# Performance work log

Hardware: AMD Instinct MI355X
Metric: run time of the kernel (lower is better)

Reference implementation:

```python
import jax, jax.numpy as jnp
import numpy as np
import math

DIM = 2048
N_HEADS = 16
N_KV_HEADS = 8
HEAD_DIM = DIM // N_HEADS  # 128
N_REP = N_HEADS // N_KV_HEADS  # 2
BLOCK = 128
TOPK = 8
NEG_INF = -10000.0
SEQ = 4096
BS = 1


def _rope_tables(seq_len, head_dim, base=10000.0):
    inv_freq = 1.0 / (base ** (jnp.arange(0, head_dim, 2, dtype=jnp.float32) / head_dim))
    ang = jnp.arange(seq_len, dtype=jnp.float32)[:, None] * inv_freq[None, :]  # [S, hd/2]
    return jnp.cos(ang), jnp.sin(ang)


def _apply_rope(t, cos, sin):
    # t: [bs, S, h, hd]; interleaved pairs
    t1 = t[..., 0::2]
    t2 = t[..., 1::2]
    c = cos[None, :, None, :]
    s = sin[None, :, None, :]
    out_even = t1 * c - t2 * s
    out_odd = t1 * s + t2 * c
    out = jnp.stack([out_even, out_odd], axis=-1)  # [bs,S,h,hd/2,2]
    return out.reshape(t.shape)


def setup_inputs() -> dict:
    key = jax.random.key(0)
    ks = jax.random.split(key, 5)
    scale = 1.0 / math.sqrt(DIM)
    x = jax.random.normal(ks[0], (BS, SEQ, DIM), dtype=jnp.float32)
    wq = jax.random.normal(ks[1], (DIM, N_HEADS * HEAD_DIM), dtype=jnp.float32) * scale
    wk = jax.random.normal(ks[2], (DIM, N_KV_HEADS * HEAD_DIM), dtype=jnp.float32) * scale
    wv = jax.random.normal(ks[3], (DIM, N_KV_HEADS * HEAD_DIM), dtype=jnp.float32) * scale
    wo = jax.random.normal(ks[4], (DIM, DIM), dtype=jnp.float32) * scale
    return {"x": x, "wq": wq, "wk": wk, "wv": wv, "wo": wo}


def reference(x, wq, wk, wv, wo):
    bs, S, _ = x.shape
    inv_sqrt_d = 1.0 / math.sqrt(HEAD_DIM)

    q = (x @ wq).reshape(bs, S, N_HEADS, HEAD_DIM)
    k = (x @ wk).reshape(bs, S, N_KV_HEADS, HEAD_DIM)
    v = (x @ wv).reshape(bs, S, N_KV_HEADS, HEAD_DIM)

    cos, sin = _rope_tables(S, HEAD_DIM)
    q = _apply_rope(q, cos, sin)
    k = _apply_rope(k, cos, sin)

    # [bs, h, S, hd]
    q = jnp.transpose(q, (0, 2, 1, 3))
    k = jnp.transpose(k, (0, 2, 1, 3))
    v = jnp.transpose(v, (0, 2, 1, 3))

    # GQA expand (repeat_interleave over head dim)
    k_e = jnp.repeat(k, N_REP, axis=1)
    v_e = jnp.repeat(v, N_REP, axis=1)

    num_blocks = S // BLOCK  # 32, divides evenly (pad_len == 0)
    k_blocks = k_e.reshape(bs, N_HEADS, num_blocks, BLOCK, HEAD_DIM)
    block_means = k_blocks.mean(axis=3)  # [bs,h,nb,hd]

    gating = jnp.einsum('bhsd,bhnd->bhsn', q, block_means) * inv_sqrt_d
    q_block_idx = jnp.arange(S) // BLOCK
    future_block = q_block_idx[:, None] < jnp.arange(num_blocks)[None, :]  # [S, nb]
    gating = jnp.where(future_block[None, None], NEG_INF, gating)

    curr_k = min(TOPK, num_blocks)
    _, sel_idx = jax.lax.top_k(gating, curr_k)  # [bs,h,S,k]
    selected = jnp.sum(jax.nn.one_hot(sel_idx, num_blocks, dtype=jnp.float32), axis=-2) > 0  # [bs,h,S,nb]

    token_keep = jnp.repeat(selected, BLOCK, axis=-1)[..., :S]  # [bs,h,S,S]
    token_mask = jnp.where(token_keep, 0.0, NEG_INF)

    scores = jnp.einsum('bhsd,bhtd->bhst', q, k_e) * inv_sqrt_d
    causal = jnp.triu(jnp.ones((S, S), dtype=jnp.float32), k=1)  # 1 where future token
    # faithful to source: elementwise max of token mask and causal*neg_inf
    final_mask = jnp.maximum(token_mask, causal[None, None] * NEG_INF)
    scores = scores + final_mask

    probs = jax.nn.softmax(scores.astype(jnp.float32), axis=-1).astype(scores.dtype)
    out = jnp.einsum('bhst,bhtd->bhsd', probs, v_e)
    out = jnp.transpose(out, (0, 2, 1, 3)).reshape(bs, S, N_HEADS * HEAD_DIM)
    return out @ wo
```

## Files before the change

kernel.cpp:

```cpp
#include <hip/hip_runtime.h>
#include <hip/hip_fp16.h>

#define SQ   4096
#define DIMM 2048
#define QKVN 4096

typedef unsigned short u16;
typedef unsigned int u32;
typedef __attribute__((ext_vector_type(8))) short    short8;
typedef __attribute__((ext_vector_type(8))) _Float16 half8;
typedef __attribute__((ext_vector_type(4))) float    f32x4;

__device__ __forceinline__ u16 f2bf(float f) {
  u32 u = __float_as_uint(f);
  u32 r = u + 0x7fffu + ((u >> 16) & 1u);
  return (u16)(r >> 16);
}
__device__ __forceinline__ float bf2f(u16 h) { return __uint_as_float(((u32)h) << 16); }
__device__ __forceinline__ u16 f2h(float f) { return __half_as_ushort(__float2half(f)); }
__device__ __forceinline__ float h2f(u16 h) { union { u16 u; _Float16 f; } c; c.u = h; return (float)c.f; }

__device__ __forceinline__ void gll16(const void* g, void* l) {
  __builtin_amdgcn_global_load_lds((const __attribute__((address_space(1))) void*)g,
                                   (__attribute__((address_space(3))) void*)l, 16, 0, 0);
}

__device__ __host__ __forceinline__ int cidx(int qb) {
  return qb < 8 ? qb : qb < 16 ? 8 + (qb - 8) * 2 : qb < 24 ? 24 + (qb - 16) * 3 : 48 + (qb - 24) * 4;
}

__global__ __launch_bounds__(256) void k_tables(float* __restrict__ cosb, float* __restrict__ sinb) {
  int idx = blockIdx.x * 256 + threadIdx.x;
  int pos = idx >> 6, i = idx & 63;
  double f = 1.0 / pow(10000.0, (double)i / 64.0);
  float inv = (float)f;
  float ang = (float)pos * inv;
  cosb[idx] = (float)cos((double)ang);
  sinb[idx] = (float)sin((double)ang);
}

__global__ __launch_bounds__(256) void k_split_x(const float* __restrict__ x,
                                                 u16* __restrict__ xh, u16* __restrict__ xl) {
  size_t base = ((size_t)blockIdx.x * 256 + threadIdx.x) * 4;
  float4 v = *(const float4*)(x + base);
  float vv[4] = {v.x, v.y, v.z, v.w};
  u16 hh[4], ll[4];
#pragma unroll
  for (int j = 0; j < 4; j++) {
    hh[j] = f2bf(vv[j]);
    ll[j] = f2bf(vv[j] - bf2f(hh[j]));
  }
  *(uint2*)(xh + base) = make_uint2((u32)hh[0] | ((u32)hh[1] << 16), (u32)hh[2] | ((u32)hh[3] << 16));
  *(uint2*)(xl + base) = make_uint2((u32)ll[0] | ((u32)ll[1] << 16), (u32)ll[2] | ((u32)ll[3] << 16));
}

__global__ __launch_bounds__(256) void k_trans_split(const float* __restrict__ src, int N,
                                                     u16* __restrict__ dh, u16* __restrict__ dl,
                                                     int rowOff) {
  __shared__ float t[64][65];
  int n0 = blockIdx.x * 64, k0 = blockIdx.y * 64;
  int tid = threadIdx.x;
  int c = tid & 63, r4 = tid >> 6;
#pragma unroll
  for (int it = 0; it < 16; it++) {
    int kk = it * 4 + r4;
    t[kk][c] = src[(size_t)(k0 + kk) * N + n0 + c];
  }
  __syncthreads();
#pragma unroll
  for (int it = 0; it < 16; it++) {
    int nn = it * 4 + r4;
    float v = t[c][nn];
    u16 hh = f2bf(v);
    size_t o = (size_t)(rowOff + n0 + nn) * 2048 + k0 + c;
    dh[o] = hh;
    dl[o] = f2bf(v - bf2f(hh));
  }
}

__global__ __launch_bounds__(256) void k_trans_f16(const float* __restrict__ src, int N,
                                                   u16* __restrict__ dst) {
  __shared__ float t[64][65];
  int n0 = blockIdx.x * 64, k0 = blockIdx.y * 64;
  int tid = threadIdx.x;
  int c = tid & 63, r4 = tid >> 6;
#pragma unroll
  for (int it = 0; it < 16; it++) {
    int kk = it * 4 + r4;
    t[kk][c] = src[(size_t)(k0 + kk) * N + n0 + c];
  }
  __syncthreads();
#pragma unroll
  for (int it = 0; it < 16; it++) {
    int nn = it * 4 + r4;
    dst[(size_t)(n0 + nn) * 2048 + k0 + c] = f2h(t[c][nn]);
  }
}

__global__ __launch_bounds__(256) void k_gemm_qkv(
    const u16* __restrict__ xh, const u16* __restrict__ xl,
    const u16* __restrict__ wth, const u16* __restrict__ wtl,
    float* __restrict__ qkv) {
  __shared__ u16 lds[4 * 128 * 64];
  const int tid = threadIdx.x;
  const int lane = tid & 63, wid = tid >> 6;
  const int rg = lane >> 4, c16 = lane & 15;
  const int bid0 = blockIdx.y * 32 + blockIdx.x;
  const int swz = (bid0 & 7) * 128 + (bid0 >> 3);
  const int m0 = (swz >> 5) * 128, n0 = (swz & 31) * 128;
  const int wm = wid >> 1, wn = wid & 1;
  const u16* gsrc = (wid == 0) ? xh + (size_t)m0 * 2048
                  : (wid == 1) ? xl + (size_t)m0 * 2048
                  : (wid == 2) ? wth + (size_t)n0 * 2048
                               : wtl + (size_t)n0 * 2048;
  u16* ldsm = lds + wid * 8192;
  const int sr = lane >> 3, scn = lane & 7;

  f32x4 acc[4][4];
#pragma unroll
  for (int a = 0; a < 4; a++)
#pragma unroll
    for (int b = 0; b < 4; b++) acc[a][b] = (f32x4){0.f, 0.f, 0.f, 0.f};

  for (int k0 = 0; k0 < 2048; k0 += 64) {
#pragma unroll
    for (int i = 0; i < 16; i++) {
      int r = i * 8 + sr;
      int cs = (scn ^ (r & 7)) * 8;
      gll16(gsrc + (size_t)r * 2048 + k0 + cs, ldsm + i * 512);
    }
    __syncthreads();
#pragma unroll
    for (int kk = 0; kk < 2; kk++) {
      short8 ah[4], al[4], bh[4], bl[4];
      int ch = kk * 4 + rg;
#pragma unroll
      for (int mf = 0; mf < 4; mf++) {
        int m = wm * 64 + mf * 16 + c16;
        int off = m * 64 + ((ch ^ (m & 7)) * 8);
        ah[mf] = *(const short8*)(lds + off);
        al[mf] = *(const short8*)(lds + 8192 + off);
      }
#pragma unroll
      for (int nf = 0; nf < 4; nf++) {
        int n = wn * 64 + nf * 16 + c16;
        int off = n * 64 + ((ch ^ (n & 7)) * 8);
        bh[nf] = *(const short8*)(lds + 16384 + off);
        bl[nf] = *(const short8*)(lds + 24576 + off);
      }
#pragma unroll
      for (int mf = 0; mf < 4; mf++)
#pragma unroll
        for (int nf = 0; nf < 4; nf++) {
          acc[mf][nf] = __builtin_amdgcn_mfma_f32_16x16x32_bf16(ah[mf], bh[nf], acc[mf][nf], 0, 0, 0);
          acc[mf][nf] = __builtin_amdgcn_mfma_f32_16x16x32_bf16(ah[mf], bl[nf], acc[mf][nf], 0, 0, 0);
          acc[mf][nf] = __builtin_amdgcn_mfma_f32_16x16x32_bf16(al[mf], bh[nf], acc[mf][nf], 0, 0, 0);
        }
    }
    __syncthreads();
  }
#pragma unroll
  for (int mf = 0; mf < 4; mf++)
#pragma unroll
    for (int nf = 0; nf < 4; nf++)
#pragma unroll
      for (int j = 0; j < 4; j++) {
        int m = m0 + wm * 64 + mf * 16 + rg * 4 + j;
        int n = n0 + wn * 64 + nf * 16 + c16;
        qkv[(size_t)m * QKVN + n] = acc[mf][nf][j];
      }
}

__global__ __launch_bounds__(256) void k_rope_qk(const float* __restrict__ qkv,
                                                 const float* __restrict__ cosb,
                                                 const float* __restrict__ sinb,
                                                 u16* __restrict__ qf, u16* __restrict__ kf2) {
  int idx = blockIdx.x * 256 + threadIdx.x;
  int i = idx & 63;
  int th = idx >> 6;
  int h = th % 24, t = th / 24;
  int c0 = (h < 16) ? h * 128 + 2 * i : 2048 + (h - 16) * 128 + 2 * i;
  float2 eo = *(const float2*)(qkv + (size_t)t * QKVN + c0);
  float c = cosb[t * 64 + i], s = sinb[t * 64 + i];
  float re = eo.x * c - eo.y * s;
  float ro = eo.x * s + eo.y * c;
  if (h < 16) {
    const float QSC = (float)(1.4426950408889634 * 0.08838834764831843);
    u32 pk = (u32)f2h(re * QSC) | ((u32)f2h(ro * QSC) << 16);
    *(u32*)(qf + ((size_t)h * SQ + t) * 128 + 2 * i) = pk;
  } else {
    int hk = h - 16;
    int d = 2 * i;
    int tile = t >> 6, tok = t & 63;
    int kk = tok >> 5, t5 = tok & 31;
    int hf = (t5 >> 2) & 1, c16v = ((t5 >> 3) << 2) | (t5 & 3);
    int dk = d >> 5, rg = (d >> 3) & 3, e = d & 7;
    int lane = rg * 16 + c16v, f = (kk * 2 + hf) * 4 + dk;
    u32 pk = (u32)f2h(re) | ((u32)f2h(ro) << 16);
    *(u32*)(kf2 + ((size_t)((hk * 64 + tile) * 16 + f) * 64 + lane) * 8 + e) = pk;
  }
}

__global__ __launch_bounds__(64) void k_bm(const float* __restrict__ qkv,
                                           const float* __restrict__ cosb,
                                           const float* __restrict__ sinb,
                                           float* __restrict__ bm) {
  int hk = blockIdx.x >> 5, n = blockIdx.x & 31;
  int i = threadIdx.x;
  double se = 0.0, so = 0.0;
  for (int t = 0; t < 128; t++) {
    int tt = n * 128 + t;
    float2 eo = *(const float2*)(qkv + (size_t)tt * QKVN + 2048 + hk * 128 + 2 * i);
    float c = cosb[tt * 64 + i], s = sinb[tt * 64 + i];
    se += (double)(eo.x * c - eo.y * s);
    so += (double)(eo.x * s + eo.y * c);
  }
  float* o = bm + ((size_t)(hk * 32 + n)) * 128 + 2 * i;
  o[0] = (float)(se * (1.0 / 128.0));
  o[1] = (float)(so * (1.0 / 128.0));
}

__global__ __launch_bounds__(64) void k_gate(const float* __restrict__ qkv,
                                             const float* __restrict__ cosb,
                                             const float* __restrict__ sinb,
                                             const float* __restrict__ bm,
                                             unsigned char* __restrict__ sel) {
  __shared__ float q[64][129];
  __shared__ float bml[32 * 128];
  int bz = blockIdx.x;
  int h = bz / 48;
  int rem = bz % 48;
  int b = 8 + (rem >> 1);
  int half = rem & 1;
  int tid = threadIdx.x;
  int hk = h >> 1;
  for (int rr = 0; rr < 64; rr++) {
    int ss = b * 128 + half * 64 + rr;
    float2 eo = *(const float2*)(qkv + (size_t)ss * QKVN + h * 128 + 2 * tid);
    float c = cosb[ss * 64 + tid], sn = sinb[ss * 64 + tid];
    q[rr][2 * tid]     = eo.x * c - eo.y * sn;
    q[rr][2 * tid + 1] = eo.x * sn + eo.y * c;
  }
  for (int o = tid; o < (b + 1) * 128; o += 64) bml[o] = bm[(size_t)hk * 32 * 128 + o];
  __syncthreads();
  int s = b * 128 + half * 64 + tid;
  double gb = 0.0;
  for (int d = 0; d < 128; d++) gb += (double)q[tid][d] * (double)bml[b * 128 + d];
  int cnt = 0;
  for (int n = 0; n < b; n++) {
    double g = 0.0;
    for (int d = 0; d < 128; d++) g += (double)q[tid][d] * (double)bml[n * 128 + d];
    cnt += (g >= gb) ? 1 : 0;
  }
  sel[h * SQ + s] = (cnt <= 7) ? 1 : 0;
}

__global__ __launch_bounds__(256) void k_vt2(const float* __restrict__ qkv, u16* __restrict__ vt2) {
  int hk = blockIdx.x & 7, tile = blockIdx.x >> 3;
  int tid = threadIdx.x;
  u16* dst = vt2 + (size_t)(hk * 64 + tile) * 8192;
#pragma unroll
  for (int rep = 0; rep < 16; rep++) {
    int idx = rep * 256 + tid;
    int tp = idx >> 7;
    int d  = idx & 127;
    int t  = tile * 64 + tp * 2;
    float v0 = qkv[(size_t)t * QKVN + 3072 + hk * 128 + d];
    float v1 = qkv[(size_t)(t + 1) * QKVN + 3072 + hk * 128 + d];
    int tok = tp * 2;
    int kk = tok >> 5, rg = (tok >> 3) & 3, e = tok & 7;
    int nf = d >> 4, c16v = d & 15;
    int lane = rg * 16 + c16v, g = kk * 8 + nf;
    u32 pk = (u32)f2h(v0) | ((u32)f2h(v1) << 16);
    *(u32*)(dst + ((size_t)(g * 64 + lane)) * 8 + e) = pk;
  }
}

__global__ __launch_bounds__(256) void k_attn_chunk(
    const u16* __restrict__ qf, const u16* __restrict__ kf2, const u16* __restrict__ vt2,
    const unsigned char* __restrict__ sel, u16* __restrict__ po, float* __restrict__ ml) {
  __shared__ u16 lds[2][8192];
  const int L = blockIdx.x;
  const int hk = L & 7;
  const int c = L >> 3;
  const int h = hk * 2 + (c & 1);
  const int cc = c >> 1;
  int qb, chunk;
  if (cc < 8)       { qb = cc;                   chunk = 0; }
  else if (cc < 24) { qb = 8 + ((cc - 8) >> 1);  chunk = (cc - 8) & 1; }
  else if (cc < 48) { qb = 16 + (cc - 24) / 3;   chunk = (cc - 24) % 3; }
  else              { qb = 24 + ((cc - 48) >> 2); chunk = (cc - 48) & 3; }
  const int nt128 = (qb < 8) ? 8 : (qb + 1);
  const int t0 = chunk * 32;
  const int t1 = (t0 + 32 < nt128 * 4) ? t0 + 32 : nt128 * 4;
  const int tid = threadIdx.x;
  const int lane = tid & 63, wid = tid >> 6;
  const int rg = lane >> 4, c16 = lane & 15;
  const bool hasMask = (qb >= 8);

  half8 aq[2][4];
#pragma unroll
  for (int mi = 0; mi < 2; mi++)
#pragma unroll
    for (int dk = 0; dk < 4; dk++) {
      int srow = qb * 128 + wid * 32 + mi * 16 + c16;
      aq[mi][dk] = *(const half8*)(qf + ((size_t)h * SQ + srow) * 128 + dk * 32 + rg * 8);
    }

  bool os2[2] = {true, true};
  if (hasMask) {
#pragma unroll
    for (int mi = 0; mi < 2; mi++)
      os2[mi] = sel[h * SQ + qb * 128 + wid * 32 + mi * 16 + c16] != 0;
  }

  f32x4 accO[2][8];
#pragma unroll
  for (int mi = 0; mi < 2; mi++)
#pragma unroll
    for (int nf = 0; nf < 8; nf++) accO[mi][nf] = (f32x4){0.f, 0.f, 0.f, 0.f};
  float mrun[2] = {-1e30f, -1e30f}, lrun[2] = {0.f, 0.f};

  const u16* kbase = kf2 + (size_t)hk * 64 * 8192;
  const u16* vbase = vt2 + (size_t)hk * 64 * 8192;

  auto stage = [&](int b, int n) {
    const u16* ks = kbase + (size_t)n * 4096;
    const u16* vs = vbase + (size_t)n * 4096;
#pragma unroll
    for (int r = 0; r < 2; r++) {
      gll16(ks + r * 2048 + wid * 512 + lane * 8, &lds[b][r * 2048 + wid * 512]);
      gll16(vs + r * 2048 + wid * 512 + lane * 8, &lds[b][4096 + r * 2048 + wid * 512]);
    }
  };

  stage(0, t0);

  for (int n = t0; n < t1; n++) {
    const int cur = (n - t0) & 1;
    __syncthreads();
    if (n + 1 < t1) stage(cur ^ 1, n + 1);
    const u16* lb = &lds[cur][0];

    f32x4 st[2][2];
#pragma unroll
    for (int hf = 0; hf < 2; hf++)
#pragma unroll
      for (int mi = 0; mi < 2; mi++) st[hf][mi] = (f32x4){0.f, 0.f, 0.f, 0.f};

    __builtin_amdgcn_s_setprio(1);
#pragma unroll
    for (int hf = 0; hf < 2; hf++) {
      half8 ka[4];
#pragma unroll
      for (int dk = 0; dk < 4; dk++)
        ka[dk] = *(const half8*)(lb + (hf * 4 + dk) * 512 + lane * 8);
#pragma unroll
      for (int dk = 0; dk < 4; dk++) {
        st[hf][0] = __builtin_amdgcn_mfma_f32_16x16x32_f16(ka[dk], aq[0][dk], st[hf][0], 0, 0, 0);
        st[hf][1] = __builtin_amdgcn_mfma_f32_16x16x32_f16(ka[dk], aq[1][dk], st[hf][1], 0, 0, 0);
      }
    }
    __builtin_amdgcn_s_setprio(0);

    if (hasMask && n >= 4 * qb) {
#pragma unroll
      for (int mi = 0; mi < 2; mi++) {
        if (!os2[mi]) {
          int row = qb * 128 + wid * 32 + mi * 16 + c16;
#pragma unroll
          for (int hf = 0; hf < 2; hf++)
#pragma unroll
            for (int j = 0; j < 4; j++) {
              int tg = n * 32 + rg * 8 + hf * 4 + j;
              if (tg > row) st[hf][mi][j] = -1e30f;
            }
        }
      }
    }

#pragma unroll
    for (int mi = 0; mi < 2; mi++) {
      float mt = st[0][mi][0];
#pragma unroll
      for (int hf = 0; hf < 2; hf++)
#pragma unroll
        for (int j = 0; j < 4; j++)
          if (hf | j) mt = fmaxf(mt, st[hf][mi][j]);
      mt = fmaxf(mt, __shfl_xor(mt, 16, 64));
      mt = fmaxf(mt, __shfl_xor(mt, 32, 64));
      if (!__all(mt <= mrun[mi] + 8.f)) {
        float mnew = fmaxf(mrun[mi], mt);
        float sc = exp2f(mrun[mi] - mnew);
        mrun[mi] = mnew;
        lrun[mi] *= sc;
#pragma unroll
        for (int nf = 0; nf < 8; nf++) accO[mi][nf] *= sc;
      }
      float ps = 0.f;
#pragma unroll
      for (int hf = 0; hf < 2; hf++)
#pragma unroll
        for (int j = 0; j < 4; j++) {
          float p = exp2f(st[hf][mi][j] - mrun[mi]);
          st[hf][mi][j] = p;
          ps += p;
        }
      ps += __shfl_xor(ps, 16, 64);
      ps += __shfl_xor(ps, 32, 64);
      lrun[mi] += ps;
    }

    half8 pa[2];
#pragma unroll
    for (int mi = 0; mi < 2; mi++) {
      union { half8 v; _Float16 e[8]; } pu;
#pragma unroll
      for (int hf = 0; hf < 2; hf++)
#pragma unroll
        for (int j = 0; j < 4; j++)
          pu.e[hf * 4 + j] = (_Float16)st[hf][mi][j];
      pa[mi] = pu.v;
    }

    __builtin_amdgcn_s_setprio(1);
#pragma unroll
    for (int nf = 0; nf < 8; nf++) {
      half8 va = *(const half8*)(lb + 4096 + nf * 512 + lane * 8);
      accO[0][nf] = __builtin_amdgcn_mfma_f32_16x16x32_f16(va, pa[0], accO[0][nf], 0, 0, 0);
      accO[1][nf] = __builtin_amdgcn_mfma_f32_16x16x32_f16(va, pa[1], accO[1][nf], 0, 0, 0);
    }
    __builtin_amdgcn_s_setprio(0);
  }

  const int pidx = h * 80 + cidx(qb) + chunk;
  u16* pob = po + (size_t)pidx * 16384;
#pragma unroll
  for (int mi = 0; mi < 2; mi++) {
    float inv = 1.0f / lrun[mi];
    int row = wid * 32 + mi * 16 + c16;
#pragma unroll
    for (int nf = 0; nf < 8; nf++) {
      u32 p0 = (u32)f2h(accO[mi][nf][0] * inv) | ((u32)f2h(accO[mi][nf][1] * inv) << 16);
      u32 p1 = (u32)f2h(accO[mi][nf][2] * inv) | ((u32)f2h(accO[mi][nf][3] * inv) << 16);
      *(uint2*)&pob[row * 128 + nf * 16 + rg * 4] = make_uint2(p0, p1);
    }
    if (rg == 0)
      ml[(size_t)pidx * 128 + row] = mrun[mi] + log2f(lrun[mi]);
  }
}

__global__ __launch_bounds__(256) void k_attn_combine(
    const u16* __restrict__ po, const float* __restrict__ ml, u16* __restrict__ attn) {
  const int qb = blockIdx.x, h = blockIdx.y;
  const int nc = (qb < 8) ? 1 : (qb < 16) ? 2 : (qb < 24) ? 3 : 4;
  const int base = h * 80 + cidx(qb);
  const int tid = threadIdx.x;
  const int r = tid >> 1, h64 = (tid & 1) * 64;
  float mp[4], M = -1e30f;
#pragma unroll
  for (int ci = 0; ci < 4; ci++) {
    mp[ci] = (ci < nc) ? ml[(size_t)(base + ci) * 128 + r] : -1e30f;
    M = fmaxf(M, mp[ci]);
  }
  float w[4], Ws = 0.f;
#pragma unroll
  for (int ci = 0; ci < 4; ci++) { w[ci] = exp2f(mp[ci] - M); Ws += (ci < nc) ? w[ci] : 0.f; }
  float inv = 1.0f / Ws;
  for (int d = 0; d < 64; d += 4) {
    float a[4] = {0.f, 0.f, 0.f, 0.f};
#pragma unroll
    for (int ci = 0; ci < 4; ci++) {
      if (ci < nc) {
        uint2 u = *(const uint2*)&po[(size_t)(base + ci) * 16384 + r * 128 + h64 + d];
        a[0] += w[ci] * h2f((u16)(u.x & 0xffff));
        a[1] += w[ci] * h2f((u16)(u.x >> 16));
        a[2] += w[ci] * h2f((u16)(u.y & 0xffff));
        a[3] += w[ci] * h2f((u16)(u.y >> 16));
      }
    }
    u32 p0 = (u32)f2h(a[0] * inv) | ((u32)f2h(a[1] * inv) << 16);
    u32 p1 = (u32)f2h(a[2] * inv) | ((u32)f2h(a[3] * inv) << 16);
    *(uint2*)&attn[(size_t)(qb * 128 + r) * DIMM + h * 128 + h64 + d] = make_uint2(p0, p1);
  }
}

__global__ __launch_bounds__(256) void k_gemm_out(
    const u16* __restrict__ attn, const u16* __restrict__ wot, float* __restrict__ out) {
  __shared__ u16 lds[2 * 128 * 64];
  const int tid = threadIdx.x;
  const int lane = tid & 63, wid = tid >> 6;
  const int rg = lane >> 4, c16 = lane & 15;
  const int bid0 = blockIdx.y * 16 + blockIdx.x;
  const int swz = (bid0 & 7) * 64 + (bid0 >> 3);
  const int m0 = (swz >> 4) * 128, n0 = (swz & 15) * 128;
  const int wm = wid >> 1, wn = wid & 1;
  const u16* gsrc = (wid < 2) ? attn + (size_t)m0 * 2048 : wot + (size_t)n0 * 2048;
  const int sr = lane >> 3, scn = lane & 7;

  f32x4 acc[4][4];
#pragma unroll
  for (int a = 0; a < 4; a++)
#pragma unroll
    for (int b = 0; b < 4; b++) acc[a][b] = (f32x4){0.f, 0.f, 0.f, 0.f};

  for (int k0 = 0; k0 < 2048; k0 += 64) {
#pragma unroll
    for (int i = 0; i < 8; i++) {
      int slot = wid * 8 + i;
      int s2 = slot & 15;
      int r = s2 * 8 + sr;
      int cs = (scn ^ (r & 7)) * 8;
      gll16(gsrc + (size_t)r * 2048 + k0 + cs, lds + slot * 512);
    }
    __syncthreads();
#pragma unroll
    for (int kk = 0; kk < 2; kk++) {
      half8 a[4], b[4];
      int ch = kk * 4 + rg;
#pragma unroll
      for (int mf = 0; mf < 4; mf++) {
        int m = wm * 64 + mf * 16 + c16;
        a[mf] = *(const half8*)(lds + m * 64 + ((ch ^ (m & 7)) * 8));
      }
#pragma unroll
      for (int nf = 0; nf < 4; nf++) {
        int n = wn * 64 + nf * 16 + c16;
        b[nf] = *(const half8*)(lds + 8192 + n * 64 + ((ch ^ (n & 7)) * 8));
      }
#pragma unroll
      for (int mf = 0; mf < 4; mf++)
#pragma unroll
        for (int nf = 0; nf < 4; nf++)
          acc[mf][nf] = __builtin_amdgcn_mfma_f32_16x16x32_f16(a[mf], b[nf], acc[mf][nf], 0, 0, 0);
    }
    __syncthreads();
  }
#pragma unroll
  for (int mf = 0; mf < 4; mf++)
#pragma unroll
    for (int nf = 0; nf < 4; nf++)
#pragma unroll
      for (int j = 0; j < 4; j++) {
        int m = m0 + wm * 64 + mf * 16 + rg * 4 + j;
        int n = n0 + wn * 64 + nf * 16 + c16;
        out[(size_t)m * DIMM + n] = acc[mf][nf][j];
      }
}

extern "C" void kernel_launch(void* const* d_in, const int* in_sizes, int n_in,
                              void* d_out, int out_size, void* d_ws, size_t ws_size,
                              hipStream_t stream) {
  (void)in_sizes; (void)n_in; (void)out_size; (void)ws_size;
  const float* x  = (const float*)d_in[0];
  const float* wq = (const float*)d_in[1];
  const float* wk = (const float*)d_in[2];
  const float* wv = (const float*)d_in[3];
  const float* wo = (const float*)d_in[4];
  float* out = (float*)d_out;

  char* ws = (char*)d_ws;
  const size_t MB = 1024 * 1024;
  char* A = ws;
  u16*   xh  = (u16*)(A);
  u16*   xl  = (u16*)(A + 16 * MB);
  u16*   wth = (u16*)(A + 32 * MB);
  u16*   wtl = (u16*)(A + 48 * MB);
  float* qkv = (float*)(A + 64 * MB);
  u16*   po  = (u16*)(A);
  float* ml  = (float*)(A + 48 * MB);
  char* B = ws + 128 * MB;
  size_t off = 0;
  auto alloc = [&](size_t b) { char* p = B + off; off += (b + 255) & ~(size_t)255; return p; };
  u16*   wot  = (u16*)alloc((size_t)DIMM * DIMM * 2);
  float* cosb = (float*)alloc((size_t)SQ * 64 * 4);
  float* sinb = (float*)alloc((size_t)SQ * 64 * 4);
  u16*   qf   = (u16*)alloc((size_t)16 * SQ * 128 * 2);
  u16*   kf2  = (u16*)alloc((size_t)8 * SQ * 128 * 2);
  u16*   vt2  = (u16*)alloc((size_t)8 * 128 * SQ * 2);
  float* bm   = (float*)alloc((size_t)8 * 32 * 128 * 4);
  unsigned char* sel = (unsigned char*)alloc((size_t)16 * SQ);
  u16*   attn = (u16*)alloc((size_t)SQ * DIMM * 2);

  k_tables<<<SQ * 64 / 256, 256, 0, stream>>>(cosb, sinb);
  k_split_x<<<(SQ * DIMM) / (256 * 4), 256, 0, stream>>>(x, xh, xl);
  k_trans_split<<<dim3(32, 32), 256, 0, stream>>>(wq, 2048, wth, wtl, 0);
  k_trans_split<<<dim3(16, 32), 256, 0, stream>>>(wk, 1024, wth, wtl, 2048);
  k_trans_split<<<dim3(16, 32), 256, 0, stream>>>(wv, 1024, wth, wtl, 3072);
  k_trans_f16<<<dim3(32, 32), 256, 0, stream>>>(wo, 2048, wot);
  k_gemm_qkv<<<dim3(32, 32), 256, 0, stream>>>(xh, xl, wth, wtl, qkv);
  k_rope_qk<<<(SQ * 24 * 64) / 256, 256, 0, stream>>>(qkv, cosb, sinb, qf, kf2);
  k_vt2<<<512, 256, 0, stream>>>(qkv, vt2);
  k_bm<<<256, 64, 0, stream>>>(qkv, cosb, sinb, bm);
  k_gate<<<16 * 48, 64, 0, stream>>>(qkv, cosb, sinb, bm, sel);
  k_attn_chunk<<<1280, 256, 0, stream>>>(qf, kf2, vt2, sel, po, ml);
  k_attn_combine<<<dim3(32, 16), 256, 0, stream>>>(po, ml, attn);
  k_gemm_out<<<dim3(16, 32), 256, 0, stream>>>(attn, wot, out);
}
```

Measured before the change: 568.6 us.

## Double-buffer LDS in QKV and output GEMMs with K=32 stages

```diff
diff --git a/kernel.cpp b/kernel.cpp
--- a/kernel.cpp
+++ b/kernel.cpp
@@ -101,7 +101,7 @@
     const u16* __restrict__ xh, const u16* __restrict__ xl,
     const u16* __restrict__ wth, const u16* __restrict__ wtl,
     float* __restrict__ qkv) {
-  __shared__ u16 lds[4 * 128 * 64];
+  __shared__ u16 lds[2][16384];
   const int tid = threadIdx.x;
   const int lane = tid & 63, wid = tid >> 6;
   const int rg = lane >> 4, c16 = lane & 15;
@@ -113,8 +113,8 @@
                   : (wid == 1) ? xl + (size_t)m0 * 2048
                   : (wid == 2) ? wth + (size_t)n0 * 2048
                                : wtl + (size_t)n0 * 2048;
-  u16* ldsm = lds + wid * 8192;
-  const int sr = lane >> 3, scn = lane & 7;
+  const int srow4 = lane >> 2;
+  const int pc = lane & 3;
 
   f32x4 acc[4][4];
 #pragma unroll
@@ -122,42 +122,47 @@
 #pragma unroll
     for (int b = 0; b < 4; b++) acc[a][b] = (f32x4){0.f, 0.f, 0.f, 0.f};
 
-  for (int k0 = 0; k0 < 2048; k0 += 64) {
-#pragma unroll
-    for (int i = 0; i < 16; i++) {
-      int r = i * 8 + sr;
-      int cs = (scn ^ (r & 7)) * 8;
-      gll16(gsrc + (size_t)r * 2048 + k0 + cs, ldsm + i * 512);
-    }
+  auto stage = [&](int b, int k0) {
+#pragma unroll
+    for (int i = 0; i < 8; i++) {
+      int r = i * 16 + srow4;
+      int cl = pc ^ ((r >> 1) & 3);
+      gll16(gsrc + (size_t)r * 2048 + k0 + cl * 8, &lds[b][wid * 4096 + i * 512 + lane * 8]);
+    }
+  };
+
+  stage(0, 0);
+
+  for (int ks = 0; ks < 64; ks++) {
     __syncthreads();
-#pragma unroll
-    for (int kk = 0; kk < 2; kk++) {
-      short8 ah[4], al[4], bh[4], bl[4];
-      int ch = kk * 4 + rg;
-#pragma unroll
-      for (int mf = 0; mf < 4; mf++) {
-        int m = wm * 64 + mf * 16 + c16;
-        int off = m * 64 + ((ch ^ (m & 7)) * 8);
-        ah[mf] = *(const short8*)(lds + off);
-        al[mf] = *(const short8*)(lds + 8192 + off);
+    if (ks + 1 < 64) stage((ks & 1) ^ 1, (ks + 1) * 32);
+    const u16* lb = lds[ks & 1];
+
+    short8 ah[4], al[4], bh[4], bl[4];
+#pragma unroll
+    for (int mf = 0; mf < 4; mf++) {
+      int m = wm * 64 + mf * 16 + c16;
+      int xo = m * 32 + ((rg ^ ((m >> 1) & 3)) * 8);
+      ah[mf] = *(const short8*)(lb + xo);
+      al[mf] = *(const short8*)(lb + 4096 + xo);
+    }
+#pragma unroll
+    for (int nf = 0; nf < 4; nf++) {
+      int n = wn * 64 + nf * 16 + c16;
+      int xo = n * 32 + ((rg ^ ((n >> 1) & 3)) * 8);
+      bh[nf] = *(const short8*)(lb + 8192 + xo);
+      bl[nf] = *(const short8*)(lb + 12288 + xo);
+    }
+    __builtin_amdgcn_s_setprio(1);
+#pragma unroll
+    for (int mf = 0; mf < 4; mf++)
+#pragma unroll
+      for (int nf = 0; nf < 4; nf++) {
+        acc[mf][nf] = __builtin_amdgcn_mfma_f32_16x16x32_bf16(ah[mf], bh[nf], acc[mf][nf], 0, 0, 0);
+        acc[mf][nf] = __builtin_amdgcn_mfma_f32_16x16x32_bf16(ah[mf], bl[nf], acc[mf][nf], 0, 0, 0);
+        acc[mf][nf] = __builtin_amdgcn_mfma_f32_16x16x32_bf16(al[mf], bh[nf], acc[mf][nf], 0, 0, 0);
       }
-#pragma unroll
-      for (int nf = 0; nf < 4; nf++) {
-        int n = wn * 64 + nf * 16 + c16;
-        int off = n * 64 + ((ch ^ (n & 7)) * 8);
-        bh[nf] = *(const short8*)(lds + 16384 + off);
-        bl[nf] = *(const short8*)(lds + 24576 + off);
-      }
-#pragma unroll
-      for (int mf = 0; mf < 4; mf++)
-#pragma unroll
-        for (int nf = 0; nf < 4; nf++) {
-          acc[mf][nf] = __builtin_amdgcn_mfma_f32_16x16x32_bf16(ah[mf], bh[nf], acc[mf][nf], 0, 0, 0);
-          acc[mf][nf] = __builtin_amdgcn_mfma_f32_16x16x32_bf16(ah[mf], bl[nf], acc[mf][nf], 0, 0, 0);
-          acc[mf][nf] = __builtin_amdgcn_mfma_f32_16x16x32_bf16(al[mf], bh[nf], acc[mf][nf], 0, 0, 0);
-        }
-    }
-    __syncthreads();
+    __builtin_amdgcn_s_setprio(0);
   }
 #pragma unroll
   for (int mf = 0; mf < 4; mf++)
@@ -487,7 +492,7 @@
 
 __global__ __launch_bounds__(256) void k_gemm_out(
     const u16* __restrict__ attn, const u16* __restrict__ wot, float* __restrict__ out) {
-  __shared__ u16 lds[2 * 128 * 64];
+  __shared__ u16 lds[2][8192];
   const int tid = threadIdx.x;
   const int lane = tid & 63, wid = tid >> 6;
   const int rg = lane >> 4, c16 = lane & 15;
@@ -496,7 +501,10 @@
   const int m0 = (swz >> 4) * 128, n0 = (swz & 15) * 128;
   const int wm = wid >> 1, wn = wid & 1;
   const u16* gsrc = (wid < 2) ? attn + (size_t)m0 * 2048 : wot + (size_t)n0 * 2048;
-  const int sr = lane >> 3, scn = lane & 7;
+  const int obase = (wid < 2) ? 0 : 4096;
+  const int i2base = (wid & 1) * 4;
+  const int srow4 = lane >> 2;
+  const int pc = lane & 3;
 
   f32x4 acc[4][4];
 #pragma unroll
@@ -504,37 +512,41 @@
 #pragma unroll
     for (int b = 0; b < 4; b++) acc[a][b] = (f32x4){0.f, 0.f, 0.f, 0.f};
 
-  for (int k0 = 0; k0 < 2048; k0 += 64) {
-#pragma unroll
-    for (int i = 0; i < 8; i++) {
-      int slot = wid * 8 + i;
-      int s2 = slot & 15;
-      int r = s2 * 8 + sr;
-      int cs = (scn ^ (r & 7)) * 8;
-      gll16(gsrc + (size_t)r * 2048 + k0 + cs, lds + slot * 512);
-    }
+  auto stage = [&](int b, int k0) {
+#pragma unroll
+    for (int i = 0; i < 4; i++) {
+      int i2 = i2base + i;
+      int r = i2 * 16 + srow4;
+      int cl = pc ^ ((r >> 1) & 3);
+      gll16(gsrc + (size_t)r * 2048 + k0 + cl * 8, &lds[b][obase + i2 * 512 + lane * 8]);
+    }
+  };
+
+  stage(0, 0);
+
+  for (int ks = 0; ks < 64; ks++) {
     __syncthreads();
-#pragma unroll
-    for (int kk = 0; kk < 2; kk++) {
-      half8 a[4], b[4];
-      int ch = kk * 4 + rg;
-#pragma unroll
-      for (int mf = 0; mf < 4; mf++) {
-        int m = wm * 64 + mf * 16 + c16;
-        a[mf] = *(const half8*)(lds + m * 64 + ((ch ^ (m & 7)) * 8));
-      }
-#pragma unroll
-      for (int nf = 0; nf < 4; nf++) {
-        int n = wn * 64 + nf * 16 + c16;
-        b[nf] = *(const half8*)(lds + 8192 + n * 64 + ((ch ^ (n & 7)) * 8));
-      }
-#pragma unroll
-      for (int mf = 0; mf < 4; mf++)
-#pragma unroll
-        for (int nf = 0; nf < 4; nf++)
-          acc[mf][nf] = __builtin_amdgcn_mfma_f32_16x16x32_f16(a[mf], b[nf], acc[mf][nf], 0, 0, 0);
-    }
-    __syncthreads();
+    if (ks + 1 < 64) stage((ks & 1) ^ 1, (ks + 1) * 32);
+    const u16* lb = lds[ks & 1];
+
+    half8 a[4], b[4];
+#pragma unroll
+    for (int mf = 0; mf < 4; mf++) {
+      int m = wm * 64 + mf * 16 + c16;
+      a[mf] = *(const half8*)(lb + m * 32 + ((rg ^ ((m >> 1) & 3)) * 8));
+    }
+#pragma unroll
+    for (int nf = 0; nf < 4; nf++) {
+      int n = wn * 64 + nf * 16 + c16;
+      b[nf] = *(const half8*)(lb + 4096 + n * 32 + ((rg ^ ((n >> 1) & 3)) * 8));
+    }
+    __builtin_amdgcn_s_setprio(1);
+#pragma unroll
+    for (int mf = 0; mf < 4; mf++)
+#pragma unroll
+      for (int nf = 0; nf < 4; nf++)
+        acc[mf][nf] = __builtin_amdgcn_mfma_f32_16x16x32_f16(a[mf], b[nf], acc[mf][nf], 0, 0, 0);
+    __builtin_amdgcn_s_setprio(0);
   }
 #pragma unroll
   for (int mf = 0; mf < 4; mf++)
```

Result: slower. 594.1 us (+4.5%).
